# Optimization experiments

Measured on AMD Instinct MI355X. Metric: run time of the kernel, lower is better.

## Reference

```python
import jax, jax.numpy as jnp
import numpy as np

B, D, H, W = 32, 256, 32, 32
K = 1024
COMMITMENT_COST = 0.25


def setup_inputs() -> dict:
    key = jax.random.key(0)
    k1, k2 = jax.random.split(key)
    z = jax.random.normal(k1, (B, D, H, W), dtype=jnp.float32)
    # torch init: uniform_(-1/K, 1/K)
    emb_weight = jax.random.uniform(k2, (K, D), dtype=jnp.float32,
                                    minval=-1.0 / K, maxval=1.0 / K)
    return {"z": z, "emb_weight": emb_weight}


def reference(z, emb_weight):
    b, c, h, w = z.shape
    # [B, D, H, W] -> [B*H*W, D]
    z_flat = jnp.transpose(z, (0, 2, 3, 1)).reshape(-1, c)
    # squared-distance: ||z||^2 + ||e||^2 - 2 z.e  -> [N, K]
    distances = (jnp.sum(z_flat ** 2, axis=1, keepdims=True)
                 + jnp.sum(emb_weight ** 2, axis=1)[None, :]
                 - 2.0 * jnp.matmul(z_flat, emb_weight.T))
    encoding_indices = jnp.argmin(distances, axis=1)  # [N]
    z_q = emb_weight[encoding_indices]                # [N, D]
    z_q = z_q.reshape(b, h, w, c).transpose(0, 3, 1, 2)  # [B, D, H, W]

    q_latent_loss = jnp.mean((jax.lax.stop_gradient(z_q) - z) ** 2)
    e_latent_loss = jnp.mean((z_q - jax.lax.stop_gradient(z)) ** 2)
    loss = q_latent_loss + COMMITMENT_COST * e_latent_loss

    # straight-through estimator
    z_q = z + jax.lax.stop_gradient(z_q - z)
    return z_q, loss, encoding_indices
```

## Files before the change

kernel.cpp:

```cpp
#include <hip/hip_runtime.h>

#define NPTS  32768
#define DIM   256

#define ZQ_OFF   0
#define LOSS_OFF 8388608
#define IDX_OFF  8388609

typedef __attribute__((ext_vector_type(8))) short short8;
typedef __attribute__((ext_vector_type(4))) float f32x4;
typedef unsigned short ushort_t;
typedef unsigned int u32;
typedef unsigned long long u64;

__device__ __forceinline__ int z_base(int n) { return ((n >> 10) << 18) | (n & 1023); }

__device__ __forceinline__ ushort_t f2bf(float f) {
    u32 u = __float_as_uint(f);
    u += 0x7FFFu + ((u >> 16) & 1u);
    return (ushort_t)(u >> 16);
}

__device__ __forceinline__ u64 pack_vi(float v, int i) {
    u32 u = __float_as_uint(v);
    u32 key = (u & 0x80000000u) ? ~u : u;
    return ((u64)key << 32) | (u32)i;
}

__device__ __forceinline__ float np_half_sq(const float* __restrict__ p, int stride) {
    float S[16];
#pragma unroll
    for (int l = 0; l < 16; ++l) {
        float t[8];
#pragma unroll
        for (int j = 0; j < 8; ++j) {
            float v = p[(j * 16 + l) * stride];
            t[j] = __fmul_rn(v, v);
        }
        S[l] = __fadd_rn(__fadd_rn(__fadd_rn(t[0], t[1]), __fadd_rn(t[2], t[3])),
                         __fadd_rn(__fadd_rn(t[4], t[5]), __fadd_rn(t[6], t[7])));
    }
    float u[8];
#pragma unroll
    for (int i = 0; i < 8; ++i) u[i] = __fadd_rn(S[i], S[i + 8]);
    float v4[4];
#pragma unroll
    for (int i = 0; i < 4; ++i) v4[i] = __fadd_rn(u[i], u[i + 4]);
    return __fadd_rn(__fadd_rn(v4[0], v4[2]), __fadd_rn(v4[1], v4[3]));
}
__device__ __forceinline__ float np_sum256_sq(const float* __restrict__ p, int stride) {
    return __fadd_rn(np_half_sq(p, stride), np_half_sq(p + 128 * stride, stride));
}

__device__ __forceinline__ float np_half_sq_abs(const float* __restrict__ p, int stride, float* aacc) {
    float S[16]; float a = *aacc;
#pragma unroll
    for (int l = 0; l < 16; ++l) {
        float t[8];
#pragma unroll
        for (int j = 0; j < 8; ++j) {
            float v = p[(j * 16 + l) * stride];
            t[j] = __fmul_rn(v, v);
            a = __fadd_rn(a, fabsf(v));
        }
        S[l] = __fadd_rn(__fadd_rn(__fadd_rn(t[0], t[1]), __fadd_rn(t[2], t[3])),
                         __fadd_rn(__fadd_rn(t[4], t[5]), __fadd_rn(t[6], t[7])));
    }
    float u[8];
#pragma unroll
    for (int i = 0; i < 8; ++i) u[i] = __fadd_rn(S[i], S[i + 8]);
    float v4[4];
#pragma unroll
    for (int i = 0; i < 4; ++i) v4[i] = __fadd_rn(u[i], u[i + 4]);
    *aacc = a;
    return __fadd_rn(__fadd_rn(v4[0], v4[2]), __fadd_rn(v4[1], v4[3]));
}

__global__ __launch_bounds__(256) void setup_kernel(
    const float* __restrict__ z, const float* __restrict__ emb,
    float* __restrict__ z2, float* __restrict__ eps,
    float* __restrict__ e2, float* __restrict__ e2h,
    ushort_t* __restrict__ ebf, u64* __restrict__ bestG,
    double* __restrict__ loss_acc, unsigned int* __restrict__ ticket)
{
    if (blockIdx.x < 128) {
        int n = blockIdx.x * 256 + threadIdx.x;
        const float* p = z + z_base(n);
        float a = 0.0f;
        float h0 = np_half_sq_abs(p, 1024, &a);
        float h1 = np_half_sq_abs(p + 128 * 1024, 1024, &a);
        z2[n] = __fadd_rn(h0, h1);
        eps[n] = __builtin_fmaf(1e-5f, a, 3e-4f);
        bestG[n] = 0x7FFFFFFFFFFFFFFFULL;
        if (blockIdx.x == 0 && threadIdx.x == 0) { *loss_acc = 0.0; *ticket = 0u; }
    } else {
        int kb = (blockIdx.x - 128) * 64;
        for (int i = threadIdx.x; i < 2048; i += 256) {
            int klocal = i >> 5, c = i & 31;
            int k = kb + klocal;
            int dt = c >> 2, lq = c & 3;
            int kt = k >> 5, nt = (k >> 4) & 1, lr = k & 15;
            const float* e = emb + k * 256 + dt * 32 + lq * 8;
            short8 ov;
#pragma unroll
            for (int j = 0; j < 8; ++j) ov[j] = (short)f2bf(e[j]);
            int f = kt * 16 + nt * 8 + dt;
            *(short8*)(ebf + (f << 9) + ((lq << 4) + lr) * 8) = ov;
        }
        if (threadIdx.x < 64) {
            int k = kb + threadIdx.x;
            float s = np_sum256_sq(emb + k * DIM, 1);
            e2[k] = s;
            e2h[k] = 0.5f * s;
        }
    }
}

__global__ __launch_bounds__(256, 4) void dist_kernel(
    const float* __restrict__ z, const float* __restrict__ emb,
    const ushort_t* __restrict__ ebf,
    const float* __restrict__ z2w, const float* __restrict__ e2w,
    const float* __restrict__ e2hw, const float* __restrict__ epsw,
    u64* __restrict__ bestG)
{
    __shared__ __align__(16) float zx[32 * 68];
    __shared__ __align__(16) int cl[2048];
    __shared__ float e2hS[1024];
    __shared__ unsigned int cntS[64];
    __shared__ int ovfS;

    const int tid = threadIdx.x;
    const int w  = tid >> 6;
    const int l  = tid & 63;
    const int lq = l >> 4;
    const int lr = l & 15;
    const int n0 = blockIdx.x << 6;
    const int zb = z_base(n0);
    const int pbase = w << 4;

    if (tid < 64) cntS[tid] = 0u;
    if (tid == 0) ovfS = 0;
    for (int i = tid; i < 1024; i += 256) e2hS[i] = e2hw[i];

    short8 af[8];
    {
        const float* zp = z + zb + pbase + lr;
#pragma unroll
        for (int dt = 0; dt < 8; ++dt)
#pragma unroll
            for (int j = 0; j < 8; ++j)
                af[dt][j] = (short)f2bf(zp[((dt << 5) + (lq << 3) + j) << 10]);
    }

    float4 epsv = *(const float4*)(epsw + n0 + pbase + (lq << 2));
    float eps_r[4] = { epsv.x, epsv.y, epsv.z, epsv.w };
    float Mr[4] = { -3.4e38f, -3.4e38f, -3.4e38f, -3.4e38f };

    __syncthreads();

    const ushort_t* fb = ebf + (l << 3);
    short8 B[2][2];
    B[0][0] = *(const short8*)(fb + (0 << 9));
    B[0][1] = *(const short8*)(fb + (8 << 9));
    B[1][0] = *(const short8*)(fb + (1 << 9));
    B[1][1] = *(const short8*)(fb + (9 << 9));

    f32x4 acc[2];
#pragma unroll
    for (int nt = 0; nt < 2; ++nt) {
        float e = e2hS[(nt << 4) + lr];
        f32x4 iv = { -e, -e, -e, -e };
        acc[nt] = iv;
    }

#pragma unroll 1
    for (int kt = 0; kt < 32; ++kt) {
        const int kt1 = (kt < 31) ? kt + 1 : 0;
#pragma unroll
        for (int dt = 0; dt < 8; ++dt) {
            const int p = dt & 1;
            __builtin_amdgcn_s_setprio(1);
            acc[0] = __builtin_amdgcn_mfma_f32_16x16x32_bf16(af[dt], B[p][0], acc[0], 0, 0, 0);
            acc[1] = __builtin_amdgcn_mfma_f32_16x16x32_bf16(af[dt], B[p][1], acc[1], 0, 0, 0);
            __builtin_amdgcn_s_setprio(0);
            const int dtn = dt + 2;
            const int fk = (dtn < 8) ? kt : kt1;
            const int f0 = fk * 16 + (dtn & 7);
            B[p][0] = *(const short8*)(fb + (f0 << 9));
            B[p][1] = *(const short8*)(fb + ((f0 + 8) << 9));
        }
        {
            float mx[4], thr[4];
#pragma unroll
            for (int r = 0; r < 4; ++r) mx[r] = fmaxf(acc[0][r], acc[1][r]);
#pragma unroll
            for (int s = 1; s <= 8; s <<= 1)
#pragma unroll
                for (int r = 0; r < 4; ++r)
                    mx[r] = fmaxf(mx[r], __shfl_xor(mx[r], s, 64));
#pragma unroll
            for (int r = 0; r < 4; ++r) {
                Mr[r] = fmaxf(Mr[r], mx[r]);
                thr[r] = Mr[r] - eps_r[r];
            }
#pragma unroll
            for (int nt = 0; nt < 2; ++nt)
#pragma unroll
                for (int r = 0; r < 4; ++r) {
                    if (acc[nt][r] >= thr[r]) {
                        int pp = pbase + lq * 4 + r;
                        int kk = (kt << 5) + (nt << 4) + lr;
                        unsigned int pos = atomicAdd(&cntS[pp], 1u);
                        if (pos < 32u) cl[pp * 32 + pos] = kk;
                        else atomicMax(&ovfS, 1);
                    }
                }
        }
        if (kt < 31) {
#pragma unroll
            for (int nt = 0; nt < 2; ++nt) {
                float e = e2hS[(kt1 << 5) + (nt << 4) + lr];
                f32x4 iv = { -e, -e, -e, -e };
                acc[nt] = iv;
            }
        }
    }
    __syncthreads();

    const int pt = tid & 63;
    const int s0 = tid >> 6;
    unsigned int nc = cntS[pt]; if (nc > 32u) nc = 32u;
    bool  act[8]; int kE[8]; float accE[8];
#pragma unroll
    for (int j = 0; j < 8; ++j) {
        unsigned int s = (unsigned int)s0 + 4u * j;
        act[j] = s < nc;
        kE[j] = act[j] ? cl[pt * 32 + s] : 0;
        accE[j] = 0.0f;
    }
#pragma unroll 1
    for (int dt = 0; dt < 8; ++dt) {
        const int dbase = dt * 32;
        __syncthreads();
        {
            int q = tid & 15, dd0 = tid >> 4;
            float4 v0 = *(const float4*)(z + zb + ((dbase + dd0) << 10) + 4 * q);
            float4 v1 = *(const float4*)(z + zb + ((dbase + dd0 + 16) << 10) + 4 * q);
            *(float4*)(zx + dd0 * 68 + 4 * q) = v0;
            *(float4*)(zx + (dd0 + 16) * 68 + 4 * q) = v1;
        }
        __syncthreads();
#pragma unroll
        for (int j = 0; j < 8; ++j) {
            if (!act[j]) continue;
            const float* er = emb + kE[j] * 256 + dbase;
            float ev[32];
#pragma unroll
            for (int c = 0; c < 8; ++c) *(float4*)(ev + 4 * c) = *(const float4*)(er + 4 * c);
            float a = accE[j];
#pragma unroll
            for (int dd = 0; dd < 32; ++dd)
                a = __builtin_fmaf(zx[dd * 68 + pt], ev[dd], a);
            accE[j] = a;
        }
    }
#pragma unroll
    for (int j = 0; j < 8; ++j) {
        if (!act[j]) continue;
        int k = kE[j];
        float t1 = __fadd_rn(z2w[n0 + pt], e2w[k]);
        float d  = __fsub_rn(t1, __fmul_rn(2.0f, accE[j]));
        atomicMin(&bestG[n0 + pt], pack_vi(d, k));
    }
    __syncthreads();

    if (ovfS) {
        for (int row = 0; row < 64; ++row) {
            if (cntS[row] <= 32u) continue;
            float fa[4] = {0.f, 0.f, 0.f, 0.f};
            for (int dt = 0; dt < 8; ++dt) {
                const int dbase = dt * 32;
                __syncthreads();
                {
                    int q = tid & 15, dd0 = tid >> 4;
                    float4 v0 = *(const float4*)(z + zb + ((dbase + dd0) << 10) + 4 * q);
                    float4 v1 = *(const float4*)(z + zb + ((dbase + dd0 + 16) << 10) + 4 * q);
                    *(float4*)(zx + dd0 * 68 + 4 * q) = v0;
                    *(float4*)(zx + (dd0 + 16) * 68 + 4 * q) = v1;
                }
                __syncthreads();
                for (int c = 0; c < 4; ++c) {
                    const float* er = emb + (tid + 256 * c) * 256 + dbase;
                    for (int dd = 0; dd < 32; ++dd)
                        fa[c] = __builtin_fmaf(zx[dd * 68 + row], er[dd], fa[c]);
                }
            }
            for (int c = 0; c < 4; ++c) {
                int k = tid + 256 * c;
                float t1 = __fadd_rn(z2w[n0 + row], e2w[k]);
                float d  = __fsub_rn(t1, __fmul_rn(2.0f, fa[c]));
                atomicMin(&bestG[n0 + row], pack_vi(d, k));
            }
            __syncthreads();
        }
    }
}

__global__ __launch_bounds__(256) void zq_loss_kernel(
    const float* __restrict__ z, const float* __restrict__ emb,
    const u64* __restrict__ bestG, float* __restrict__ zq,
    double* __restrict__ loss_acc, unsigned int* __restrict__ ticket,
    float* __restrict__ out_loss, float* __restrict__ out_idx)
{
    const int tl = threadIdx.x & 63;
    const int q  = threadIdx.x >> 6;
    const int n  = blockIdx.x * 64 + tl;
    const int kk = (int)(u32)(bestG[n] & 0xFFFFFFFFULL);
    if (q == 0) out_idx[n] = (float)kk;
    const float4* er4 = (const float4*)(emb + kk * DIM + (q << 6));
    const int zb2 = z_base(n) + (q << 16);
    double s = 0.0;
#pragma unroll 4
    for (int c = 0; c < 16; ++c) {
        float4 e4 = er4[c];
#pragma unroll
        for (int j = 0; j < 4; ++j) {
            int dd = c * 4 + j;
            float ev = (j == 0) ? e4.x : (j == 1) ? e4.y : (j == 2) ? e4.z : e4.w;
            float zv = z[zb2 + (dd << 10)];
            zq[zb2 + (dd << 10)] = ev;
            float df = ev - zv;
            s = fma((double)df, (double)df, s);
        }
    }
    for (int off = 32; off; off >>= 1) s += __shfl_down(s, off, 64);
    __shared__ double sred[4];
    if ((threadIdx.x & 63) == 0) sred[threadIdx.x >> 6] = s;
    __syncthreads();
    if (threadIdx.x == 0) {
        atomicAdd(loss_acc, (sred[0] + sred[1]) + (sred[2] + sred[3]));
        __threadfence();
        unsigned int old = atomicAdd(ticket, 1u);
        if (old == gridDim.x - 1) {
            double total = atomicAdd(loss_acc, 0.0);
            out_loss[0] = (float)(1.25 * (total / 8388608.0));
        }
    }
}

extern "C" void kernel_launch(void* const* d_in, const int* in_sizes, int n_in,
                              void* d_out, int out_size, void* d_ws, size_t ws_size,
                              hipStream_t stream) {
    const float* z   = (const float*)d_in[0];
    const float* emb = (const float*)d_in[1];
    float* out = (float*)d_out;

    float* z2w = (float*)d_ws;
    float* epsw = (float*)((char*)d_ws + 131072);
    float* e2w = (float*)((char*)d_ws + 262144);
    float* e2hw = (float*)((char*)d_ws + 266240);
    ushort_t* ebf = (ushort_t*)((char*)d_ws + 270336);
    double* loss_acc = (double*)((char*)d_ws + 794624);
    unsigned int* ticket = (unsigned int*)((char*)d_ws + 794632);
    u64* bestG = (u64*)((char*)d_ws + 794640);

    setup_kernel<<<144, 256, 0, stream>>>(z, emb, z2w, epsw, e2w, e2hw, ebf,
                                          bestG, loss_acc, ticket);
    dist_kernel<<<NPTS / 64, 256, 0, stream>>>(z, emb, ebf, z2w, e2w, e2hw,
                                               epsw, bestG);
    zq_loss_kernel<<<NPTS / 64, 256, 0, stream>>>(z, emb, bestG, out + ZQ_OFF,
                                                  loss_acc, ticket,
                                                  out + LOSS_OFF, out + IDX_OFF);
}
```

Measured before the change: 218.1 us.

## Split codebook across waves with 16 points per block in dist kernel

Restructures the distance kernel so each block handles 16 points and its four waves each scan a quarter of the codebook, launching four times as many blocks. This reduces per-wave MFMA serial length and improves occupancy/parallelism across CUs. It repeats the bf16 conversion of z in every wave and uses per-wave running maxima for candidate thresholds, which can admit more candidates and trigger the overflow path more often. The setup kernel is also re-gridded to use more, smaller blocks for the z-norm pass.

```diff
diff --git a/kernel.cpp b/kernel.cpp
--- a/kernel.cpp
+++ b/kernel.cpp
@@ -12,6 +12,8 @@
 typedef unsigned short ushort_t;
 typedef unsigned int u32;
 typedef unsigned long long u64;
+
+#define ZXP 20
 
 __device__ __forceinline__ int z_base(int n) { return ((n >> 10) << 18) | (n & 1023); }
 
@@ -83,18 +85,20 @@
     ushort_t* __restrict__ ebf, u64* __restrict__ bestG,
     double* __restrict__ loss_acc, unsigned int* __restrict__ ticket)
 {
-    if (blockIdx.x < 128) {
-        int n = blockIdx.x * 256 + threadIdx.x;
-        const float* p = z + z_base(n);
-        float a = 0.0f;
-        float h0 = np_half_sq_abs(p, 1024, &a);
-        float h1 = np_half_sq_abs(p + 128 * 1024, 1024, &a);
-        z2[n] = __fadd_rn(h0, h1);
-        eps[n] = __builtin_fmaf(1e-5f, a, 3e-4f);
-        bestG[n] = 0x7FFFFFFFFFFFFFFFULL;
+    if (blockIdx.x < 256) {
+        if (threadIdx.x < 128) {
+            int n = blockIdx.x * 128 + threadIdx.x;
+            const float* p = z + z_base(n);
+            float a = 0.0f;
+            float h0 = np_half_sq_abs(p, 1024, &a);
+            float h1 = np_half_sq_abs(p + 128 * 1024, 1024, &a);
+            z2[n] = __fadd_rn(h0, h1);
+            eps[n] = __builtin_fmaf(1e-5f, a, 3e-4f);
+            bestG[n] = 0x7FFFFFFFFFFFFFFFULL;
+        }
         if (blockIdx.x == 0 && threadIdx.x == 0) { *loss_acc = 0.0; *ticket = 0u; }
     } else {
-        int kb = (blockIdx.x - 128) * 64;
+        int kb = (blockIdx.x - 256) * 64;
         for (int i = threadIdx.x; i < 2048; i += 256) {
             int klocal = i >> 5, c = i & 31;
             int k = kb + klocal;
@@ -123,28 +127,27 @@
     const float* __restrict__ e2hw, const float* __restrict__ epsw,
     u64* __restrict__ bestG)
 {
-    __shared__ __align__(16) float zx[32 * 68];
-    __shared__ __align__(16) int cl[2048];
+    __shared__ __align__(16) float zx[32 * ZXP];
+    __shared__ __align__(16) int cl[512];
     __shared__ float e2hS[1024];
-    __shared__ unsigned int cntS[64];
+    __shared__ unsigned int cntS[16];
     __shared__ int ovfS;
 
     const int tid = threadIdx.x;
-    const int w  = tid >> 6;
+    const int kq = tid >> 6;
     const int l  = tid & 63;
     const int lq = l >> 4;
     const int lr = l & 15;
-    const int n0 = blockIdx.x << 6;
+    const int n0 = blockIdx.x << 4;
     const int zb = z_base(n0);
-    const int pbase = w << 4;
-
-    if (tid < 64) cntS[tid] = 0u;
+
+    if (tid < 16) cntS[tid] = 0u;
     if (tid == 0) ovfS = 0;
     for (int i = tid; i < 1024; i += 256) e2hS[i] = e2hw[i];
 
     short8 af[8];
     {
-        const float* zp = z + zb + pbase + lr;
+        const float* zp = z + zb + lr;
 #pragma unroll
         for (int dt = 0; dt < 8; ++dt)
 #pragma unroll
@@ -152,30 +155,31 @@
                 af[dt][j] = (short)f2bf(zp[((dt << 5) + (lq << 3) + j) << 10]);
     }
 
-    float4 epsv = *(const float4*)(epsw + n0 + pbase + (lq << 2));
+    float4 epsv = *(const float4*)(epsw + n0 + (lq << 2));
     float eps_r[4] = { epsv.x, epsv.y, epsv.z, epsv.w };
     float Mr[4] = { -3.4e38f, -3.4e38f, -3.4e38f, -3.4e38f };
 
     __syncthreads();
 
     const ushort_t* fb = ebf + (l << 3);
+    const int ktg0 = kq << 3;
     short8 B[2][2];
-    B[0][0] = *(const short8*)(fb + (0 << 9));
-    B[0][1] = *(const short8*)(fb + (8 << 9));
-    B[1][0] = *(const short8*)(fb + (1 << 9));
-    B[1][1] = *(const short8*)(fb + (9 << 9));
+    B[0][0] = *(const short8*)(fb + ((ktg0 * 16 + 0) << 9));
+    B[0][1] = *(const short8*)(fb + ((ktg0 * 16 + 8) << 9));
+    B[1][0] = *(const short8*)(fb + ((ktg0 * 16 + 1) << 9));
+    B[1][1] = *(const short8*)(fb + ((ktg0 * 16 + 9) << 9));
 
     f32x4 acc[2];
 #pragma unroll
     for (int nt = 0; nt < 2; ++nt) {
-        float e = e2hS[(nt << 4) + lr];
+        float e = e2hS[(ktg0 << 5) + (nt << 4) + lr];
         f32x4 iv = { -e, -e, -e, -e };
         acc[nt] = iv;
     }
 
 #pragma unroll 1
-    for (int kt = 0; kt < 32; ++kt) {
-        const int kt1 = (kt < 31) ? kt + 1 : 0;
+    for (int kt = 0; kt < 8; ++kt) {
+        const int ktg = ktg0 + kt;
 #pragma unroll
         for (int dt = 0; dt < 8; ++dt) {
             const int p = dt & 1;
@@ -183,11 +187,11 @@
             acc[0] = __builtin_amdgcn_mfma_f32_16x16x32_bf16(af[dt], B[p][0], acc[0], 0, 0, 0);
             acc[1] = __builtin_amdgcn_mfma_f32_16x16x32_bf16(af[dt], B[p][1], acc[1], 0, 0, 0);
             __builtin_amdgcn_s_setprio(0);
-            const int dtn = dt + 2;
-            const int fk = (dtn < 8) ? kt : kt1;
-            const int f0 = fk * 16 + (dtn & 7);
-            B[p][0] = *(const short8*)(fb + (f0 << 9));
-            B[p][1] = *(const short8*)(fb + ((f0 + 8) << 9));
+            const int ndt = (dt + 2) & 7;
+            const int nktg = (dt >= 6) ? ((ktg + 1) & 31) : ktg;
+            const int nf0 = nktg * 16 + ndt;
+            B[p][0] = *(const short8*)(fb + (nf0 << 9));
+            B[p][1] = *(const short8*)(fb + ((nf0 + 8) << 9));
         }
         {
             float mx[4], thr[4];
@@ -208,18 +212,18 @@
 #pragma unroll
                 for (int r = 0; r < 4; ++r) {
                     if (acc[nt][r] >= thr[r]) {
-                        int pp = pbase + lq * 4 + r;
-                        int kk = (kt << 5) + (nt << 4) + lr;
+                        int pp = lq * 4 + r;
+                        int kk = (ktg << 5) + (nt << 4) + lr;
                         unsigned int pos = atomicAdd(&cntS[pp], 1u);
                         if (pos < 32u) cl[pp * 32 + pos] = kk;
                         else atomicMax(&ovfS, 1);
                     }
                 }
         }
-        if (kt < 31) {
+        if (kt < 7) {
 #pragma unroll
             for (int nt = 0; nt < 2; ++nt) {
-                float e = e2hS[(kt1 << 5) + (nt << 4) + lr];
+                float e = e2hS[((ktg + 1) << 5) + (nt << 4) + lr];
                 f32x4 iv = { -e, -e, -e, -e };
                 acc[nt] = iv;
             }
@@ -227,13 +231,13 @@
     }
     __syncthreads();
 
-    const int pt = tid & 63;
-    const int s0 = tid >> 6;
+    const int pt = tid & 15;
+    const int s0 = tid >> 4;
     unsigned int nc = cntS[pt]; if (nc > 32u) nc = 32u;
-    bool  act[8]; int kE[8]; float accE[8];
-#pragma unroll
-    for (int j = 0; j < 8; ++j) {
-        unsigned int s = (unsigned int)s0 + 4u * j;
+    bool  act[2]; int kE[2]; float accE[2];
+#pragma unroll
+    for (int j = 0; j < 2; ++j) {
+        unsigned int s = (unsigned int)s0 + 16u * j;
         act[j] = s < nc;
         kE[j] = act[j] ? cl[pt * 32 + s] : 0;
         accE[j] = 0.0f;
@@ -242,16 +246,14 @@
     for (int dt = 0; dt < 8; ++dt) {
         const int dbase = dt * 32;
         __syncthreads();
-        {
-            int q = tid & 15, dd0 = tid >> 4;
-            float4 v0 = *(const float4*)(z + zb + ((dbase + dd0) << 10) + 4 * q);
-            float4 v1 = *(const float4*)(z + zb + ((dbase + dd0 + 16) << 10) + 4 * q);
-            *(float4*)(zx + dd0 * 68 + 4 * q) = v0;
-            *(float4*)(zx + (dd0 + 16) * 68 + 4 * q) = v1;
+        if (tid < 128) {
+            int q = tid & 3, dd = tid >> 2;
+            float4 v = *(const float4*)(z + zb + ((dbase + dd) << 10) + 4 * q);
+            *(float4*)(zx + dd * ZXP + 4 * q) = v;
         }
         __syncthreads();
 #pragma unroll
-        for (int j = 0; j < 8; ++j) {
+        for (int j = 0; j < 2; ++j) {
             if (!act[j]) continue;
             const float* er = emb + kE[j] * 256 + dbase;
             float ev[32];
@@ -260,12 +262,12 @@
             float a = accE[j];
 #pragma unroll
             for (int dd = 0; dd < 32; ++dd)
-                a = __builtin_fmaf(zx[dd * 68 + pt], ev[dd], a);
+                a = __builtin_fmaf(zx[dd * ZXP + pt], ev[dd], a);
             accE[j] = a;
         }
     }
 #pragma unroll
-    for (int j = 0; j < 8; ++j) {
+    for (int j = 0; j < 2; ++j) {
         if (!act[j]) continue;
         int k = kE[j];
         float t1 = __fadd_rn(z2w[n0 + pt], e2w[k]);
@@ -275,24 +277,22 @@
     __syncthreads();
 
     if (ovfS) {
-        for (int row = 0; row < 64; ++row) {
+        for (int row = 0; row < 16; ++row) {
             if (cntS[row] <= 32u) continue;
             float fa[4] = {0.f, 0.f, 0.f, 0.f};
             for (int dt = 0; dt < 8; ++dt) {
                 const int dbase = dt * 32;
                 __syncthreads();
-                {
-                    int q = tid & 15, dd0 = tid >> 4;
-                    float4 v0 = *(const float4*)(z + zb + ((dbase + dd0) << 10) + 4 * q);
-                    float4 v1 = *(const float4*)(z + zb + ((dbase + dd0 + 16) << 10) + 4 * q);
-                    *(float4*)(zx + dd0 * 68 + 4 * q) = v0;
-                    *(float4*)(zx + (dd0 + 16) * 68 + 4 * q) = v1;
+                if (tid < 128) {
+                    int q = tid & 3, dd = tid >> 2;
+                    float4 v = *(const float4*)(z + zb + ((dbase + dd) << 10) + 4 * q);
+                    *(float4*)(zx + dd * ZXP + 4 * q) = v;
                 }
                 __syncthreads();
                 for (int c = 0; c < 4; ++c) {
                     const float* er = emb + (tid + 256 * c) * 256 + dbase;
                     for (int dd = 0; dd < 32; ++dd)
-                        fa[c] = __builtin_fmaf(zx[dd * 68 + row], er[dd], fa[c]);
+                        fa[c] = __builtin_fmaf(zx[dd * ZXP + row], er[dd], fa[c]);
                 }
             }
             for (int c = 0; c < 4; ++c) {
@@ -364,9 +364,9 @@
     unsigned int* ticket = (unsigned int*)((char*)d_ws + 794632);
     u64* bestG = (u64*)((char*)d_ws + 794640);
 
-    setup_kernel<<<144, 256, 0, stream>>>(z, emb, z2w, epsw, e2w, e2hw, ebf,
+    setup_kernel<<<272, 256, 0, stream>>>(z, emb, z2w, epsw, e2w, e2hw, ebf,
                                           bestG, loss_acc, ticket);
-    dist_kernel<<<NPTS / 64, 256, 0, stream>>>(z, emb, ebf, z2w, e2w, e2hw,
+    dist_kernel<<<NPTS / 16, 256, 0, stream>>>(z, emb, ebf, z2w, e2w, e2hw,
                                                epsw, bestG);
     zq_loss_kernel<<<NPTS / 64, 256, 0, stream>>>(z, emb, bestG, out + ZQ_OFF,
                                                   loss_acc, ticket,
```

Result: slower. 454.8 us (+108.5%).

## Fuse z-norm setup and zq/loss epilogue into the distance kernel

Applied to the files above, without the earlier changes.

Moves the per-point squared-norm and eps computation from the setup kernel into each dist_kernel block, keeps the per-point best (distance, index) in shared memory instead of global atomics, and folds the zq gather and loss reduction into the end of dist_kernel. This removes one kernel launch and the global round-trips for z2, eps and bestG. The setup kernel now only converts the codebook. Occupancy hint drops from 4 to 2 blocks per CU, and the epilogue adds serial work at the tail of each distance block.

```diff
diff --git a/kernel.cpp b/kernel.cpp
--- a/kernel.cpp
+++ b/kernel.cpp
@@ -77,56 +77,49 @@
 }
 
 __global__ __launch_bounds__(256) void setup_kernel(
-    const float* __restrict__ z, const float* __restrict__ emb,
-    float* __restrict__ z2, float* __restrict__ eps,
+    const float* __restrict__ emb,
     float* __restrict__ e2, float* __restrict__ e2h,
-    ushort_t* __restrict__ ebf, u64* __restrict__ bestG,
+    ushort_t* __restrict__ ebf,
     double* __restrict__ loss_acc, unsigned int* __restrict__ ticket)
 {
-    if (blockIdx.x < 128) {
-        int n = blockIdx.x * 256 + threadIdx.x;
-        const float* p = z + z_base(n);
-        float a = 0.0f;
-        float h0 = np_half_sq_abs(p, 1024, &a);
-        float h1 = np_half_sq_abs(p + 128 * 1024, 1024, &a);
-        z2[n] = __fadd_rn(h0, h1);
-        eps[n] = __builtin_fmaf(1e-5f, a, 3e-4f);
-        bestG[n] = 0x7FFFFFFFFFFFFFFFULL;
-        if (blockIdx.x == 0 && threadIdx.x == 0) { *loss_acc = 0.0; *ticket = 0u; }
-    } else {
-        int kb = (blockIdx.x - 128) * 64;
-        for (int i = threadIdx.x; i < 2048; i += 256) {
-            int klocal = i >> 5, c = i & 31;
-            int k = kb + klocal;
-            int dt = c >> 2, lq = c & 3;
-            int kt = k >> 5, nt = (k >> 4) & 1, lr = k & 15;
-            const float* e = emb + k * 256 + dt * 32 + lq * 8;
-            short8 ov;
-#pragma unroll
-            for (int j = 0; j < 8; ++j) ov[j] = (short)f2bf(e[j]);
-            int f = kt * 16 + nt * 8 + dt;
-            *(short8*)(ebf + (f << 9) + ((lq << 4) + lr) * 8) = ov;
-        }
-        if (threadIdx.x < 64) {
-            int k = kb + threadIdx.x;
-            float s = np_sum256_sq(emb + k * DIM, 1);
-            e2[k] = s;
-            e2h[k] = 0.5f * s;
-        }
-    }
-}
-
-__global__ __launch_bounds__(256, 4) void dist_kernel(
+    int kb = blockIdx.x * 8;
+    if (threadIdx.x < 256) {
+        int i = threadIdx.x;
+        int klocal = i >> 5, c = i & 31;
+        int k = kb + klocal;
+        int dt = c >> 2, lq = c & 3;
+        int kt = k >> 5, nt = (k >> 4) & 1, lr = k & 15;
+        const float* e = emb + k * 256 + dt * 32 + lq * 8;
+        short8 ov;
+#pragma unroll
+        for (int j = 0; j < 8; ++j) ov[j] = (short)f2bf(e[j]);
+        int f = kt * 16 + nt * 8 + dt;
+        *(short8*)(ebf + (f << 9) + ((lq << 4) + lr) * 8) = ov;
+    }
+    if (threadIdx.x < 8) {
+        int k = kb + threadIdx.x;
+        float s = np_sum256_sq(emb + k * DIM, 1);
+        e2[k] = s;
+        e2h[k] = 0.5f * s;
+    }
+    if (blockIdx.x == 0 && threadIdx.x == 0) { *loss_acc = 0.0; *ticket = 0u; }
+}
+
+__global__ __launch_bounds__(256, 2) void dist_kernel(
     const float* __restrict__ z, const float* __restrict__ emb,
     const ushort_t* __restrict__ ebf,
-    const float* __restrict__ z2w, const float* __restrict__ e2w,
-    const float* __restrict__ e2hw, const float* __restrict__ epsw,
-    u64* __restrict__ bestG)
+    const float* __restrict__ e2w, const float* __restrict__ e2hw,
+    float* __restrict__ zq, float* __restrict__ out_idx,
+    float* __restrict__ out_loss,
+    double* __restrict__ loss_acc, unsigned int* __restrict__ ticket)
 {
     __shared__ __align__(16) float zx[32 * 68];
     __shared__ __align__(16) int cl[2048];
     __shared__ float e2hS[1024];
+    __shared__ float z2S[64], epsS[64];
     __shared__ unsigned int cntS[64];
+    __shared__ u64 bestS[64];
+    __shared__ double sred[4];
     __shared__ int ovfS;
 
     const int tid = threadIdx.x;
@@ -138,9 +131,24 @@
     const int zb = z_base(n0);
     const int pbase = w << 4;
 
-    if (tid < 64) cntS[tid] = 0u;
+    if (tid < 64) { cntS[tid] = 0u; bestS[tid] = 0x7FFFFFFFFFFFFFFFULL; }
     if (tid == 0) ovfS = 0;
     for (int i = tid; i < 1024; i += 256) e2hS[i] = e2hw[i];
+
+    float* hbuf = (float*)cl;
+    float* abuf = hbuf + 64;
+    float hs = 0.0f, aa = 0.0f;
+    if (tid < 128) {
+        const int tl = tid & 63, half = tid >> 6;
+        aa = 0.0f;
+        hs = np_half_sq_abs(z + zb + tl + (half << 17), 1024, &aa);
+        if (half) { hbuf[tl] = hs; abuf[tl] = aa; }
+    }
+    __syncthreads();
+    if (tid < 64) {
+        z2S[tid] = __fadd_rn(hs, hbuf[tid]);
+        epsS[tid] = __builtin_fmaf(1e-5f, aa + abuf[tid], 3e-4f);
+    }
 
     short8 af[8];
     {
@@ -151,12 +159,6 @@
             for (int j = 0; j < 8; ++j)
                 af[dt][j] = (short)f2bf(zp[((dt << 5) + (lq << 3) + j) << 10]);
     }
-
-    float4 epsv = *(const float4*)(epsw + n0 + pbase + (lq << 2));
-    float eps_r[4] = { epsv.x, epsv.y, epsv.z, epsv.w };
-    float Mr[4] = { -3.4e38f, -3.4e38f, -3.4e38f, -3.4e38f };
-
-    __syncthreads();
 
     const ushort_t* fb = ebf + (l << 3);
     short8 B[2][2];
@@ -164,6 +166,15 @@
     B[0][1] = *(const short8*)(fb + (8 << 9));
     B[1][0] = *(const short8*)(fb + (1 << 9));
     B[1][1] = *(const short8*)(fb + (9 << 9));
+
+    __syncthreads();
+
+    float eps_r[4], Mr[4];
+#pragma unroll
+    for (int r = 0; r < 4; ++r) {
+        eps_r[r] = epsS[pbase + lq * 4 + r];
+        Mr[r] = -3.4e38f;
+    }
 
     f32x4 acc[2];
 #pragma unroll
@@ -268,9 +279,9 @@
     for (int j = 0; j < 8; ++j) {
         if (!act[j]) continue;
         int k = kE[j];
-        float t1 = __fadd_rn(z2w[n0 + pt], e2w[k]);
+        float t1 = __fadd_rn(z2S[pt], e2w[k]);
         float d  = __fsub_rn(t1, __fmul_rn(2.0f, accE[j]));
-        atomicMin(&bestG[n0 + pt], pack_vi(d, k));
+        atomicMin(&bestS[pt], pack_vi(d, k));
     }
     __syncthreads();
 
@@ -297,53 +308,47 @@
             }
             for (int c = 0; c < 4; ++c) {
                 int k = tid + 256 * c;
-                float t1 = __fadd_rn(z2w[n0 + row], e2w[k]);
+                float t1 = __fadd_rn(z2S[row], e2w[k]);
                 float d  = __fsub_rn(t1, __fmul_rn(2.0f, fa[c]));
-                atomicMin(&bestG[n0 + row], pack_vi(d, k));
+                atomicMin(&bestS[row], pack_vi(d, k));
             }
             __syncthreads();
         }
     }
-}
-
-__global__ __launch_bounds__(256) void zq_loss_kernel(
-    const float* __restrict__ z, const float* __restrict__ emb,
-    const u64* __restrict__ bestG, float* __restrict__ zq,
-    double* __restrict__ loss_acc, unsigned int* __restrict__ ticket,
-    float* __restrict__ out_loss, float* __restrict__ out_idx)
-{
-    const int tl = threadIdx.x & 63;
-    const int q  = threadIdx.x >> 6;
-    const int n  = blockIdx.x * 64 + tl;
-    const int kk = (int)(u32)(bestG[n] & 0xFFFFFFFFULL);
-    if (q == 0) out_idx[n] = (float)kk;
-    const float4* er4 = (const float4*)(emb + kk * DIM + (q << 6));
-    const int zb2 = z_base(n) + (q << 16);
-    double s = 0.0;
+    __syncthreads();
+
+    {
+        const int tl = tid & 63;
+        const int q  = tid >> 6;
+        const int kk = (int)(u32)(bestS[tl] & 0xFFFFFFFFULL);
+        if (q == 0) out_idx[n0 + tl] = (float)kk;
+        const float4* er4 = (const float4*)(emb + kk * DIM + (q << 6));
+        const int zb2 = zb + tl + (q << 16);
+        double s = 0.0;
 #pragma unroll 4
-    for (int c = 0; c < 16; ++c) {
-        float4 e4 = er4[c];
-#pragma unroll
-        for (int j = 0; j < 4; ++j) {
-            int dd = c * 4 + j;
-            float ev = (j == 0) ? e4.x : (j == 1) ? e4.y : (j == 2) ? e4.z : e4.w;
-            float zv = z[zb2 + (dd << 10)];
-            zq[zb2 + (dd << 10)] = ev;
-            float df = ev - zv;
-            s = fma((double)df, (double)df, s);
-        }
-    }
-    for (int off = 32; off; off >>= 1) s += __shfl_down(s, off, 64);
-    __shared__ double sred[4];
-    if ((threadIdx.x & 63) == 0) sred[threadIdx.x >> 6] = s;
-    __syncthreads();
-    if (threadIdx.x == 0) {
-        atomicAdd(loss_acc, (sred[0] + sred[1]) + (sred[2] + sred[3]));
-        __threadfence();
-        unsigned int old = atomicAdd(ticket, 1u);
-        if (old == gridDim.x - 1) {
-            double total = atomicAdd(loss_acc, 0.0);
-            out_loss[0] = (float)(1.25 * (total / 8388608.0));
+        for (int c = 0; c < 16; ++c) {
+            float4 e4 = er4[c];
+#pragma unroll
+            for (int j = 0; j < 4; ++j) {
+                int dd = c * 4 + j;
+                float ev = (j == 0) ? e4.x : (j == 1) ? e4.y : (j == 2) ? e4.z : e4.w;
+                float zv = z[zb2 + (dd << 10)];
+                zq[zb2 + (dd << 10)] = ev;
+                float df = ev - zv;
+                s = fma((double)df, (double)df, s);
+            }
+        }
+        for (int off = 32; off; off >>= 1) s += __shfl_down(s, off, 64);
+        if ((tid & 63) == 0) sred[tid >> 6] = s;
+        __syncthreads();
+        if (tid == 0) {
+            atomicAdd(loss_acc, (sred[0] + sred[1]) + (sred[2] + sred[3]));
+            __threadfence();
+            unsigned int old = atomicAdd(ticket, 1u);
+            if (old == gridDim.x - 1) {
+                double total = atomicAdd(loss_acc, 0.0);
+                out_loss[0] = (float)(1.25 * (total / 8388608.0));
+            }
         }
     }
 }
@@ -355,20 +360,14 @@
     const float* emb = (const float*)d_in[1];
     float* out = (float*)d_out;
 
-    float* z2w = (float*)d_ws;
-    float* epsw = (float*)((char*)d_ws + 131072);
     float* e2w = (float*)((char*)d_ws + 262144);
     float* e2hw = (float*)((char*)d_ws + 266240);
     ushort_t* ebf = (ushort_t*)((char*)d_ws + 270336);
     double* loss_acc = (double*)((char*)d_ws + 794624);
     unsigned int* ticket = (unsigned int*)((char*)d_ws + 794632);
-    u64* bestG = (u64*)((char*)d_ws + 794640);
-
-    setup_kernel<<<144, 256, 0, stream>>>(z, emb, z2w, epsw, e2w, e2hw, ebf,
-                                          bestG, loss_acc, ticket);
-    dist_kernel<<<NPTS / 64, 256, 0, stream>>>(z, emb, ebf, z2w, e2w, e2hw,
-                                               epsw, bestG);
-    zq_loss_kernel<<<NPTS / 64, 256, 0, stream>>>(z, emb, bestG, out + ZQ_OFF,
-                                                  loss_acc, ticket,
-                                                  out + LOSS_OFF, out + IDX_OFF);
-}
+
+    setup_kernel<<<128, 256, 0, stream>>>(emb, e2w, e2hw, ebf, loss_acc, ticket);
+    dist_kernel<<<NPTS / 64, 256, 0, stream>>>(z, emb, ebf, e2w, e2hw,
+                                               out + ZQ_OFF, out + IDX_OFF,
+                                               out + LOSS_OFF, loss_acc, ticket);
+}
```

Result: faster. 202.0 us (-7.4%).
